# Performance work log

Hardware: AMD Instinct MI355X
Metric: run time of the kernel (lower is better)

The kernel has to match this reference:

```python
import jax, jax.numpy as jnp
import numpy as np

TOP_K = 4  # config.num_experts_per_tok


def setup_inputs() -> dict:
    key = jax.random.key(0)
    ks = jax.random.split(key, 8)
    B, S, H = 1, 2048, 1024
    E, I = 16, 512          # n_routed_experts, moe_intermediate_size
    SI = 512 * 2            # shared expert intermediate = moe_inter * n_shared_experts
    w = 0.02                # weight init scale
    return {
        "hidden_states": jax.random.normal(ks[0], (B, S, H), jnp.float32),
        "gate_w": jax.random.normal(ks[1], (E, H), jnp.float32) * w,
        "expert_gate": jax.random.normal(ks[2], (E, H, I), jnp.float32) * w,
        "expert_up": jax.random.normal(ks[3], (E, H, I), jnp.float32) * w,
        "expert_down": jax.random.normal(ks[4], (E, I, H), jnp.float32) * w,
        "shared_gate": jax.random.normal(ks[5], (H, SI), jnp.float32) * w,
        "shared_up": jax.random.normal(ks[6], (H, SI), jnp.float32) * w,
        "shared_down": jax.random.normal(ks[7], (SI, H), jnp.float32) * w,
    }


def reference(hidden_states, gate_w, expert_gate, expert_up, expert_down,
              shared_gate, shared_up, shared_down):
    B, S, H = hidden_states.shape
    E = gate_w.shape[0]
    x = hidden_states.reshape(-1, H)                     # [T, H]
    T = x.shape[0]

    # ---- MoEGate: sigmoid scores, top-k, normalize weights ----
    scores = jax.nn.sigmoid(x @ gate_w.T)                # [T, E]
    topk_w, topk_idx = jax.lax.top_k(scores, TOP_K)      # [T, k]
    topk_w = topk_w / (topk_w.sum(-1, keepdims=True) + 1e-20)

    # dense combine matrix: combine[t, e] = sum_k topk_w[t,k] * (topk_idx[t,k]==e)
    combine = jnp.zeros((T, E), x.dtype).at[
        jnp.arange(T)[:, None], topk_idx].add(topk_w)    # [T, E]

    # ---- routed experts (SwiGLU), computed densely and masked by combine ----
    g = jax.nn.silu(jnp.einsum('th,ehi->tei', x, expert_gate))
    u = jnp.einsum('th,ehi->tei', x, expert_up)
    expert_out = jnp.einsum('tei,eih->teh', g * u, expert_down)  # [T, E, H]
    y = jnp.einsum('te,teh->th', combine, expert_out)    # weighted combine

    # ---- shared expert (SwiGLU on all tokens) ----
    sg = jax.nn.silu(x @ shared_gate)
    shared_out = (sg * (x @ shared_up)) @ shared_down    # [T, H]

    return (y + shared_out).reshape(B, S, H)
```

## Files before the change

kernel.cpp:

```cpp
#include <hip/hip_runtime.h>


#define T_TOK 2048
#define H_DIM 1024
#define E_NUM 16
#define I_DIM 512
#define SI_DIM 1024

typedef __bf16 bf16x8 __attribute__((ext_vector_type(8)));
typedef short short8 __attribute__((ext_vector_type(8)));
typedef float f32x4 __attribute__((ext_vector_type(4)));
typedef unsigned short u16;

struct alignas(8) U16x4 { u16 x, y, z, w; };
struct alignas(4) U16x2 { u16 x, y; };

__device__ __forceinline__ float bf2f(u16 u) {
    union { float f; unsigned int i; } v; v.i = ((unsigned int)u) << 16; return v.f;
}
__device__ __forceinline__ u16 f2bf(float f) {
    union { float f; unsigned int i; } v; v.f = f;
    unsigned int i = v.i;
    return (u16)((i + 0x7fffu + ((i >> 16) & 1u)) >> 16);
}

#define GLOAD16(g, l)                                                          \
    __builtin_amdgcn_global_load_lds(                                          \
        (const __attribute__((address_space(1))) unsigned int*)(const void*)(g),\
        (__attribute__((address_space(3))) unsigned int*)(void*)(l), 16, 0, 0)

#define CNT(e) ((e) * 16)

__global__ __launch_bounds__(256) void route_kernel(
    const float* __restrict__ x, const float* __restrict__ gw,
    int* __restrict__ cnt, int* __restrict__ tok,
    int* __restrict__ slot, float* __restrict__ wgt)
{
    const int wid  = threadIdx.x >> 6;
    const int lane = threadIdx.x & 63;
    const int t    = blockIdx.x * 4 + wid;

    const float* xp = x + (long)t * H_DIM;
    float xr[16];
#pragma unroll
    for (int j = 0; j < 16; ++j) xr[j] = xp[lane + 64 * j];

    float sc[E_NUM];
#pragma unroll
    for (int e = 0; e < E_NUM; ++e) {
        const float* gp = gw + e * H_DIM;
        float d = 0.f;
#pragma unroll
        for (int j = 0; j < 16; ++j) d += xr[j] * gp[lane + 64 * j];
#pragma unroll
        for (int off = 32; off; off >>= 1) d += __shfl_xor(d, off);
        sc[e] = 1.f / (1.f + expf(-d));
    }

    float w[4]; int id[4];
    unsigned picked = 0;
    float sum = 0.f;
#pragma unroll
    for (int k = 0; k < 4; ++k) {
        float mv = -1.f; int mi = 0;
#pragma unroll
        for (int e = 0; e < E_NUM; ++e) {
            bool ok = !((picked >> e) & 1u) && (sc[e] > mv);
            mv = ok ? sc[e] : mv;
            mi = ok ? e : mi;
        }
        w[k] = mv; id[k] = mi; picked |= 1u << mi; sum += mv;
    }
    const float inv = 1.f / (sum + 1e-20f);

    if (lane == 0) {
#pragma unroll
        for (int k = 0; k < 4; ++k) {
            int pos = atomicAdd(&cnt[CNT(id[k])], 1);
            tok[id[k] * T_TOK + pos] = t;
            slot[t * 4 + k] = (id[k] << 16) | pos;
            wgt[t * 4 + k]  = w[k] * inv;
        }
    }
}

__global__ void scan_kernel(const int* __restrict__ cnt, int* __restrict__ ebase)
{
    if (threadIdx.x == 0) {
        int s = 0;
        for (int e = 0; e < E_NUM; ++e) { ebase[e] = s; s += cnt[CNT(e)]; }
    }
}

__global__ __launch_bounds__(256) void convert_kernel(
    const float* __restrict__ in, u16* __restrict__ out)
{
    const int i = (blockIdx.x * 256 + threadIdx.x) * 4;
    float4 v = *(const float4*)&in[i];
    U16x4 o = { f2bf(v.x), f2bf(v.y), f2bf(v.z), f2bf(v.w) };
    *(U16x4*)&out[i] = o;
}

__global__ __launch_bounds__(256) void transpose_cv(
    const float* __restrict__ in, u16* __restrict__ out, int R, int C)
{
    __shared__ float tl[64][65];
    const long boff = (long)blockIdx.z * R * C;
    const int r0 = blockIdx.y * 64, c0 = blockIdx.x * 64;
    const int tid = threadIdx.x;

#pragma unroll
    for (int p = 0; p < 16; ++p) {
        int row = p * 4 + (tid >> 6), col = tid & 63;
        tl[row][col] = in[boff + (long)(r0 + row) * C + (c0 + col)];
    }
    __syncthreads();
#pragma unroll
    for (int p = 0; p < 8; ++p) {
        int cc = p * 8 + (tid >> 5), rp = (tid & 31) * 2;
        U16x2 o = { f2bf(tl[rp][cc]), f2bf(tl[rp + 1][cc]) };
        *(U16x2*)&out[boff + (long)(c0 + cc) * R + (r0 + rp)] = o;
    }
}

template<bool DUAL, bool GATHER, bool OUTF32>
__global__ __launch_bounds__(256) void gemm_bf16(
    const u16* __restrict__ A, const u16* __restrict__ B1,
    const u16* __restrict__ B2, void* __restrict__ Out,
    const int* __restrict__ cnt, const int* __restrict__ ebase,
    const int* __restrict__ tok, int Mfixed, int K, int Ntot, long sB)
{
    const int e  = blockIdx.z;
    const int M  = cnt ? cnt[CNT(e)] : Mfixed;
    const int m0 = blockIdx.y * 128;
    if (m0 >= M) return;
    const int n0 = blockIdx.x * 64;
    const int rbase = ebase ? ebase[e] : 0;
    const u16* b1p = B1 + (long)e * sB;
    const u16* b2p = DUAL ? (B2 + (long)e * sB) : B1;

    __shared__ __attribute__((aligned(16))) u16 sA[128 * 64];
    __shared__ __attribute__((aligned(16))) u16 sB1t[64 * 64];
    __shared__ __attribute__((aligned(16))) u16 sB2t[DUAL ? 64 * 64 : 8];

    const int tid  = threadIdx.x;
    const int lane = tid & 63;
    const int wid  = tid >> 6;
    const int wr   = wid >> 1;
    const int wc   = wid & 1;

    const u16* aptr[4];
#pragma unroll
    for (int i = 0; i < 4; ++i) {
        int q = i * 256 + tid;
        int row = q >> 3, s = q & 7;
        int r = m0 + row; if (r >= M) r = M - 1;
        long grow = GATHER ? (long)tok[e * T_TOK + r] : (long)(rbase + r);
        aptr[i] = A + grow * K + ((s ^ (row & 7)) << 3);
    }
    const u16* bptr1[2]; const u16* bptr2[2];
#pragma unroll
    for (int i = 0; i < 2; ++i) {
        int q = i * 256 + tid;
        int row = q >> 3, s = q & 7;
        long go = (long)(n0 + row) * K + ((s ^ (row & 7)) << 3);
        bptr1[i] = b1p + go;
        bptr2[i] = b2p + go;
    }

    f32x4 accG[4][2], accU[4][2];
#pragma unroll
    for (int i = 0; i < 4; ++i)
#pragma unroll
        for (int j = 0; j < 2; ++j) {
            accG[i][j] = (f32x4){0.f, 0.f, 0.f, 0.f};
            if (DUAL) accU[i][j] = (f32x4){0.f, 0.f, 0.f, 0.f};
        }

    for (int kt = 0; kt < K; kt += 64) {
        __syncthreads();
#pragma unroll
        for (int i = 0; i < 4; ++i) GLOAD16(aptr[i] + kt, &sA[(i * 256 + tid) * 8]);
#pragma unroll
        for (int i = 0; i < 2; ++i) {
            GLOAD16(bptr1[i] + kt, &sB1t[(i * 256 + tid) * 8]);
            if (DUAL) GLOAD16(bptr2[i] + kt, &sB2t[(i * 256 + tid) * 8]);
        }
        asm volatile("s_waitcnt vmcnt(0)" ::: "memory");
        __syncthreads();

#pragma unroll
        for (int ks = 0; ks < 2; ++ks) {
            bf16x8 a[4], bg[2], bu[2];
#pragma unroll
            for (int mf = 0; mf < 4; ++mf) {
                int row = wr * 64 + mf * 16 + (lane & 15);
                int c   = ks * 4 + (lane >> 4);
                a[mf] = __builtin_bit_cast(bf16x8,
                    *(const short8*)&sA[row * 64 + ((c ^ (row & 7)) << 3)]);
            }
#pragma unroll
            for (int nf = 0; nf < 2; ++nf) {
                int row = wc * 32 + nf * 16 + (lane & 15);
                int c   = ks * 4 + (lane >> 4);
                int o   = row * 64 + ((c ^ (row & 7)) << 3);
                bg[nf] = __builtin_bit_cast(bf16x8, *(const short8*)&sB1t[o]);
                if (DUAL) bu[nf] = __builtin_bit_cast(bf16x8, *(const short8*)&sB2t[o]);
            }
#pragma unroll
            for (int mf = 0; mf < 4; ++mf)
#pragma unroll
                for (int nf = 0; nf < 2; ++nf) {
                    accG[mf][nf] = __builtin_amdgcn_mfma_f32_16x16x32_bf16(
                        a[mf], bg[nf], accG[mf][nf], 0, 0, 0);
                    if (DUAL)
                        accU[mf][nf] = __builtin_amdgcn_mfma_f32_16x16x32_bf16(
                            a[mf], bu[nf], accU[mf][nf], 0, 0, 0);
                }
        }
    }

#pragma unroll
    for (int mf = 0; mf < 4; ++mf)
#pragma unroll
        for (int nf = 0; nf < 2; ++nf)
#pragma unroll
            for (int r = 0; r < 4; ++r) {
                int row = m0 + wr * 64 + mf * 16 + (lane >> 4) * 4 + r;
                if (row >= M) continue;
                int col = n0 + wc * 32 + nf * 16 + (lane & 15);
                float v = accG[mf][nf][r];
                if constexpr (DUAL) {
                    float uu = accU[mf][nf][r];
                    v = v / (1.f + expf(-v)) * uu;
                }
                long oidx = (long)(rbase + row) * Ntot + col;
                if constexpr (OUTF32) ((float*)Out)[oidx] = v;
                else                  ((u16*)Out)[oidx]   = f2bf(v);
            }
}

__global__ __launch_bounds__(256) void combine_kernel(
    float* __restrict__ out, const u16* __restrict__ pair,
    const int* __restrict__ slot, const float* __restrict__ wgt,
    const int* __restrict__ ebase)
{
    const int t = blockIdx.x;
    const int c = threadIdx.x * 4;
    float4 o = *(float4*)&out[(long)t * H_DIM + c];
#pragma unroll
    for (int k = 0; k < 4; ++k) {
        int s = slot[t * 4 + k];
        int e = s >> 16, pos = s & 0xffff;
        float w = wgt[t * 4 + k];
        const u16* pr = pair + (long)(ebase[e] + pos) * H_DIM + c;
        U16x4 pv = *(const U16x4*)pr;
        o.x += w * bf2f(pv.x);
        o.y += w * bf2f(pv.y);
        o.z += w * bf2f(pv.z);
        o.w += w * bf2f(pv.w);
    }
    *(float4*)&out[(long)t * H_DIM + c] = o;
}

extern "C" void kernel_launch(void* const* d_in, const int* in_sizes, int n_in,
                              void* d_out, int out_size, void* d_ws, size_t ws_size,
                              hipStream_t stream)
{
    const float* x  = (const float*)d_in[0];
    const float* gw = (const float*)d_in[1];
    const float* eg = (const float*)d_in[2];
    const float* eu = (const float*)d_in[3];
    const float* ed = (const float*)d_in[4];
    const float* sg = (const float*)d_in[5];
    const float* su = (const float*)d_in[6];
    const float* sd = (const float*)d_in[7];
    float* out = (float*)d_out;

    unsigned char* w = (unsigned char*)d_ws;
    size_t off = 0;
    auto alloc = [&](size_t b) -> void* {
        off = (off + 255) & ~(size_t)255;
        void* p = w + off; off += b; return p;
    };
    int*   cnt   = (int*)  alloc(256 * 4);
    int*   ebase = (int*)  alloc(16 * 4);
    int*   tok   = (int*)  alloc((size_t)E_NUM * T_TOK * 4);
    int*   slot  = (int*)  alloc((size_t)T_TOK * 4 * 4);
    float* wgt   = (float*)alloc((size_t)T_TOK * 4 * 4);
    u16*   xb    = (u16*)  alloc((size_t)T_TOK * H_DIM * 2);
    u16*   egT   = (u16*)  alloc((size_t)E_NUM * I_DIM * H_DIM * 2);
    u16*   euT   = (u16*)  alloc((size_t)E_NUM * I_DIM * H_DIM * 2);
    u16*   edT   = (u16*)  alloc((size_t)E_NUM * H_DIM * I_DIM * 2);
    u16*   sgT   = (u16*)  alloc((size_t)SI_DIM * H_DIM * 2);
    u16*   suT   = (u16*)  alloc((size_t)SI_DIM * H_DIM * 2);
    u16*   sdT   = (u16*)  alloc((size_t)H_DIM * SI_DIM * 2);
    u16*   actR  = (u16*)  alloc((size_t)T_TOK * 4 * I_DIM * 2);
    u16*   actS  = (u16*)  alloc((size_t)T_TOK * SI_DIM * 2);
    u16*   pair  = (u16*)  alloc((size_t)T_TOK * 4 * H_DIM * 2);

    hipMemsetAsync(cnt, 0, 256 * 4, stream);

    route_kernel<<<T_TOK / 4, 256, 0, stream>>>(x, gw, cnt, tok, slot, wgt);
    scan_kernel<<<1, 64, 0, stream>>>(cnt, ebase);

    convert_kernel<<<T_TOK * H_DIM / 1024, 256, 0, stream>>>(x, xb);
    transpose_cv<<<dim3(I_DIM / 64, H_DIM / 64, E_NUM), 256, 0, stream>>>(eg, egT, H_DIM, I_DIM);
    transpose_cv<<<dim3(I_DIM / 64, H_DIM / 64, E_NUM), 256, 0, stream>>>(eu, euT, H_DIM, I_DIM);
    transpose_cv<<<dim3(H_DIM / 64, I_DIM / 64, E_NUM), 256, 0, stream>>>(ed, edT, I_DIM, H_DIM);
    transpose_cv<<<dim3(16, 16, 1), 256, 0, stream>>>(sg, sgT, H_DIM, SI_DIM);
    transpose_cv<<<dim3(16, 16, 1), 256, 0, stream>>>(su, suT, H_DIM, SI_DIM);
    transpose_cv<<<dim3(16, 16, 1), 256, 0, stream>>>(sd, sdT, SI_DIM, H_DIM);

    gemm_bf16<true, true, false><<<dim3(I_DIM / 64, 16, E_NUM), 256, 0, stream>>>(
        xb, egT, euT, actR, cnt, ebase, tok, 0, H_DIM, I_DIM, (long)I_DIM * H_DIM);
    gemm_bf16<true, false, false><<<dim3(SI_DIM / 64, T_TOK / 128, 1), 256, 0, stream>>>(
        xb, sgT, suT, actS, nullptr, nullptr, nullptr, T_TOK, H_DIM, SI_DIM, 0);
    gemm_bf16<false, false, false><<<dim3(H_DIM / 64, 16, E_NUM), 256, 0, stream>>>(
        actR, edT, nullptr, pair, cnt, ebase, nullptr, 0, I_DIM, H_DIM, (long)H_DIM * I_DIM);
    gemm_bf16<false, false, true><<<dim3(H_DIM / 64, T_TOK / 128, 1), 256, 0, stream>>>(
        actS, sdT, nullptr, out, nullptr, nullptr, nullptr, T_TOK, SI_DIM, H_DIM, 0);

    combine_kernel<<<T_TOK, 256, 0, stream>>>(out, pair, slot, wgt, ebase);
}
```

Before: 291.0 us.

## Merge launches into fused transpose and grouped GEMM kernels with double-buffered LDS

Measured after the change: 351.4 us. +20.8%, slower.

```diff
diff --git a/kernel.cpp b/kernel.cpp
--- a/kernel.cpp
+++ b/kernel.cpp
@@ -34,7 +34,7 @@
 __global__ __launch_bounds__(256) void route_kernel(
     const float* __restrict__ x, const float* __restrict__ gw,
     int* __restrict__ cnt, int* __restrict__ tok,
-    int* __restrict__ slot, float* __restrict__ wgt)
+    int* __restrict__ slot, float* __restrict__ wgt, u16* __restrict__ xb)
 {
     const int wid  = threadIdx.x >> 6;
     const int lane = threadIdx.x & 63;
@@ -44,6 +44,9 @@
     float xr[16];
 #pragma unroll
     for (int j = 0; j < 16; ++j) xr[j] = xp[lane + 64 * j];
+
+#pragma unroll
+    for (int j = 0; j < 16; ++j) xb[(long)t * H_DIM + lane + 64 * j] = f2bf(xr[j]);
 
     float sc[E_NUM];
 #pragma unroll
@@ -84,29 +87,13 @@
     }
 }
 
-__global__ void scan_kernel(const int* __restrict__ cnt, int* __restrict__ ebase)
-{
-    if (threadIdx.x == 0) {
-        int s = 0;
-        for (int e = 0; e < E_NUM; ++e) { ebase[e] = s; s += cnt[CNT(e)]; }
-    }
-}
-
-__global__ __launch_bounds__(256) void convert_kernel(
-    const float* __restrict__ in, u16* __restrict__ out)
-{
-    const int i = (blockIdx.x * 256 + threadIdx.x) * 4;
-    float4 v = *(const float4*)&in[i];
-    U16x4 o = { f2bf(v.x), f2bf(v.y), f2bf(v.z), f2bf(v.w) };
-    *(U16x4*)&out[i] = o;
-}
-
-__global__ __launch_bounds__(256) void transpose_cv(
-    const float* __restrict__ in, u16* __restrict__ out, int R, int C)
+__device__ __forceinline__ void tr_tile(
+    const float* __restrict__ in, u16* __restrict__ out,
+    int R, int C, int z, int by, int bx)
 {
     __shared__ float tl[64][65];
-    const long boff = (long)blockIdx.z * R * C;
-    const int r0 = blockIdx.y * 64, c0 = blockIdx.x * 64;
+    const long boff = (long)z * R * C;
+    const int r0 = by * 64, c0 = bx * 64;
     const int tid = threadIdx.x;
 
 #pragma unroll
@@ -123,25 +110,90 @@
     }
 }
 
-template<bool DUAL, bool GATHER, bool OUTF32>
-__global__ __launch_bounds__(256) void gemm_bf16(
-    const u16* __restrict__ A, const u16* __restrict__ B1,
-    const u16* __restrict__ B2, void* __restrict__ Out,
-    const int* __restrict__ cnt, const int* __restrict__ ebase,
-    const int* __restrict__ tok, int Mfixed, int K, int Ntot, long sB)
-{
-    const int e  = blockIdx.z;
-    const int M  = cnt ? cnt[CNT(e)] : Mfixed;
-    const int m0 = blockIdx.y * 128;
+__global__ __launch_bounds__(256) void transpose_mega(
+    const float* __restrict__ eg, const float* __restrict__ eu,
+    const float* __restrict__ ed, const float* __restrict__ sg,
+    const float* __restrict__ su, const float* __restrict__ sd,
+    u16* __restrict__ egT, u16* __restrict__ euT, u16* __restrict__ edT,
+    u16* __restrict__ sgT, u16* __restrict__ suT, u16* __restrict__ sdT)
+{
+    int b = blockIdx.x;
+    if (b < 2048) {
+        int z = b >> 7, rem = b & 127;
+        tr_tile(eg, egT, H_DIM, I_DIM, z, rem >> 3, rem & 7);
+    } else if (b < 4096) {
+        int l = b - 2048; int z = l >> 7, rem = l & 127;
+        tr_tile(eu, euT, H_DIM, I_DIM, z, rem >> 3, rem & 7);
+    } else if (b < 6144) {
+        int l = b - 4096; int z = l >> 7, rem = l & 127;
+        tr_tile(ed, edT, I_DIM, H_DIM, z, rem >> 4, rem & 15);
+    } else if (b < 6400) {
+        int l = b - 6144;
+        tr_tile(sg, sgT, H_DIM, SI_DIM, 0, l >> 4, l & 15);
+    } else if (b < 6656) {
+        int l = b - 6400;
+        tr_tile(su, suT, H_DIM, SI_DIM, 0, l >> 4, l & 15);
+    } else {
+        int l = b - 6656;
+        tr_tile(sd, sdT, SI_DIM, H_DIM, 0, l >> 4, l & 15);
+    }
+}
+
+template<int MODE>
+__global__ __launch_bounds__(256) void gemm_moe(
+    const u16* __restrict__ xb, const u16* __restrict__ actR,
+    const u16* __restrict__ actS,
+    const u16* __restrict__ Wr1, const u16* __restrict__ Wr2,
+    const u16* __restrict__ Ws1, const u16* __restrict__ Ws2,
+    u16* __restrict__ outR, void* __restrict__ outS,
+    const int* __restrict__ cnt, const int* __restrict__ tok)
+{
+    constexpr bool DUAL  = (MODE == 0);
+    constexpr int  NWG   = (MODE == 0) ? 2304 : 4352;
+    constexpr int  CPX   = NWG / 8;
+    constexpr int  RB    = (MODE == 0) ? 2048 : 4096;
+    constexpr int  PER_E = RB / E_NUM;
+
+    const int bswz = blockIdx.x;
+    const int idx  = (bswz & 7) * CPX + (bswz >> 3);
+
+    const bool routed = idx < RB;
+    int e = 0, mb, nb;
+    if (routed) {
+        e = idx / PER_E;
+        int rem = idx % PER_E;
+        nb = rem >> 4;
+        mb = rem & 15;
+    } else {
+        int rem = idx - RB;
+        nb = rem >> 4;
+        mb = rem & 15;
+    }
+
+    int M, K, Ntot, rbase = 0;
+    const u16 *Ap, *B1p, *B2p = nullptr;
+    if (routed) {
+        M = cnt[CNT(e)];
+#pragma unroll
+        for (int i = 0; i < E_NUM; ++i) rbase += (i < e) ? cnt[CNT(i)] : 0;
+        K    = (MODE == 0) ? H_DIM : I_DIM;
+        Ntot = (MODE == 0) ? I_DIM : H_DIM;
+        Ap   = (MODE == 0) ? xb : actR;
+        B1p  = Wr1 + (long)e * (512L * 1024L);
+        if (DUAL) B2p = Wr2 + (long)e * (512L * 1024L);
+    } else {
+        M = T_TOK; K = (MODE == 0) ? H_DIM : SI_DIM;
+        Ntot = (MODE == 0) ? SI_DIM : H_DIM;
+        Ap = (MODE == 0) ? xb : actS;
+        B1p = Ws1; if (DUAL) B2p = Ws2;
+    }
+    const int m0 = mb * 128;
     if (m0 >= M) return;
-    const int n0 = blockIdx.x * 64;
-    const int rbase = ebase ? ebase[e] : 0;
-    const u16* b1p = B1 + (long)e * sB;
-    const u16* b2p = DUAL ? (B2 + (long)e * sB) : B1;
-
-    __shared__ __attribute__((aligned(16))) u16 sA[128 * 64];
-    __shared__ __attribute__((aligned(16))) u16 sB1t[64 * 64];
-    __shared__ __attribute__((aligned(16))) u16 sB2t[DUAL ? 64 * 64 : 8];
+    const int n0 = nb * 64;
+
+    __shared__ __attribute__((aligned(16))) u16 sA[2][128 * 64];
+    __shared__ __attribute__((aligned(16))) u16 sB1[2][64 * 64];
+    __shared__ __attribute__((aligned(16))) u16 sB2[DUAL ? 2 : 1][DUAL ? 64 * 64 : 8];
 
     const int tid  = threadIdx.x;
     const int lane = tid & 63;
@@ -155,8 +207,11 @@
         int q = i * 256 + tid;
         int row = q >> 3, s = q & 7;
         int r = m0 + row; if (r >= M) r = M - 1;
-        long grow = GATHER ? (long)tok[e * T_TOK + r] : (long)(rbase + r);
-        aptr[i] = A + grow * K + ((s ^ (row & 7)) << 3);
+        long grow;
+        if (MODE == 0 && routed) grow = tok[e * T_TOK + r];
+        else if (routed)         grow = rbase + r;
+        else                     grow = r;
+        aptr[i] = Ap + grow * (long)K + ((s ^ (row & 7)) << 3);
     }
     const u16* bptr1[2]; const u16* bptr2[2];
 #pragma unroll
@@ -164,8 +219,8 @@
         int q = i * 256 + tid;
         int row = q >> 3, s = q & 7;
         long go = (long)(n0 + row) * K + ((s ^ (row & 7)) << 3);
-        bptr1[i] = b1p + go;
-        bptr2[i] = b2p + go;
+        bptr1[i] = B1p + go;
+        bptr2[i] = DUAL ? (B2p + go) : B1p;
     }
 
     f32x4 accG[4][2], accU[4][2];
@@ -177,18 +232,28 @@
             if (DUAL) accU[i][j] = (f32x4){0.f, 0.f, 0.f, 0.f};
         }
 
-    for (int kt = 0; kt < K; kt += 64) {
-        __syncthreads();
-#pragma unroll
-        for (int i = 0; i < 4; ++i) GLOAD16(aptr[i] + kt, &sA[(i * 256 + tid) * 8]);
+    auto STAGE = [&](int buf, int kt) {
+#pragma unroll
+        for (int i = 0; i < 4; ++i) GLOAD16(aptr[i] + kt, &sA[buf][(i * 256 + tid) * 8]);
 #pragma unroll
         for (int i = 0; i < 2; ++i) {
-            GLOAD16(bptr1[i] + kt, &sB1t[(i * 256 + tid) * 8]);
-            if (DUAL) GLOAD16(bptr2[i] + kt, &sB2t[(i * 256 + tid) * 8]);
-        }
-        asm volatile("s_waitcnt vmcnt(0)" ::: "memory");
-        __syncthreads();
-
+            GLOAD16(bptr1[i] + kt, &sB1[buf][(i * 256 + tid) * 8]);
+            if (DUAL) GLOAD16(bptr2[i] + kt, &sB2[buf][(i * 256 + tid) * 8]);
+        }
+    };
+
+    const int nt = K >> 6;
+    STAGE(0, 0);
+    asm volatile("s_waitcnt vmcnt(0)" ::: "memory");
+    __syncthreads();
+
+    int cur = 0;
+    for (int t = 0; t < nt; ++t) {
+        if (t + 1 < nt) STAGE(cur ^ 1, (t + 1) << 6);
+
+        const u16* sAc  = sA[cur];
+        const u16* sB1c = sB1[cur];
+        const u16* sB2c = sB2[DUAL ? cur : 0];
 #pragma unroll
         for (int ks = 0; ks < 2; ++ks) {
             bf16x8 a[4], bg[2], bu[2];
@@ -197,15 +262,15 @@
                 int row = wr * 64 + mf * 16 + (lane & 15);
                 int c   = ks * 4 + (lane >> 4);
                 a[mf] = __builtin_bit_cast(bf16x8,
-                    *(const short8*)&sA[row * 64 + ((c ^ (row & 7)) << 3)]);
+                    *(const short8*)&sAc[row * 64 + ((c ^ (row & 7)) << 3)]);
             }
 #pragma unroll
             for (int nf = 0; nf < 2; ++nf) {
                 int row = wc * 32 + nf * 16 + (lane & 15);
                 int c   = ks * 4 + (lane >> 4);
                 int o   = row * 64 + ((c ^ (row & 7)) << 3);
-                bg[nf] = __builtin_bit_cast(bf16x8, *(const short8*)&sB1t[o]);
-                if (DUAL) bu[nf] = __builtin_bit_cast(bf16x8, *(const short8*)&sB2t[o]);
+                bg[nf] = __builtin_bit_cast(bf16x8, *(const short8*)&sB1c[o]);
+                if (DUAL) bu[nf] = __builtin_bit_cast(bf16x8, *(const short8*)&sB2c[o]);
             }
 #pragma unroll
             for (int mf = 0; mf < 4; ++mf)
@@ -218,6 +283,12 @@
                             a[mf], bu[nf], accU[mf][nf], 0, 0, 0);
                 }
         }
+
+        if (t + 1 < nt) {
+            asm volatile("s_waitcnt vmcnt(0)" ::: "memory");
+            __syncthreads();
+        }
+        cur ^= 1;
     }
 
 #pragma unroll
@@ -234,17 +305,26 @@
                     float uu = accU[mf][nf][r];
                     v = v / (1.f + expf(-v)) * uu;
                 }
-                long oidx = (long)(rbase + row) * Ntot + col;
-                if constexpr (OUTF32) ((float*)Out)[oidx] = v;
-                else                  ((u16*)Out)[oidx]   = f2bf(v);
+                long orow = routed ? (long)(rbase + row) : (long)row;
+                if (MODE == 1 && !routed) ((float*)outS)[orow * Ntot + col] = v;
+                else if (routed)          outR[orow * Ntot + col] = f2bf(v);
+                else                      ((u16*)outS)[orow * Ntot + col] = f2bf(v);
             }
 }
 
 __global__ __launch_bounds__(256) void combine_kernel(
     float* __restrict__ out, const u16* __restrict__ pair,
     const int* __restrict__ slot, const float* __restrict__ wgt,
-    const int* __restrict__ ebase)
-{
+    const int* __restrict__ cnt)
+{
+    __shared__ int eb_s[E_NUM];
+    if (threadIdx.x < E_NUM) {
+        int s = 0;
+        for (int i = 0; i < E_NUM; ++i) s += (i < (int)threadIdx.x) ? cnt[CNT(i)] : 0;
+        eb_s[threadIdx.x] = s;
+    }
+    __syncthreads();
+
     const int t = blockIdx.x;
     const int c = threadIdx.x * 4;
     float4 o = *(float4*)&out[(long)t * H_DIM + c];
@@ -253,7 +333,7 @@
         int s = slot[t * 4 + k];
         int e = s >> 16, pos = s & 0xffff;
         float w = wgt[t * 4 + k];
-        const u16* pr = pair + (long)(ebase[e] + pos) * H_DIM + c;
+        const u16* pr = pair + (long)(eb_s[e] + pos) * H_DIM + c;
         U16x4 pv = *(const U16x4*)pr;
         o.x += w * bf2f(pv.x);
         o.y += w * bf2f(pv.y);
@@ -283,43 +363,31 @@
         off = (off + 255) & ~(size_t)255;
         void* p = w + off; off += b; return p;
     };
-    int*   cnt   = (int*)  alloc(256 * 4);
-    int*   ebase = (int*)  alloc(16 * 4);
-    int*   tok   = (int*)  alloc((size_t)E_NUM * T_TOK * 4);
-    int*   slot  = (int*)  alloc((size_t)T_TOK * 4 * 4);
-    float* wgt   = (float*)alloc((size_t)T_TOK * 4 * 4);
-    u16*   xb    = (u16*)  alloc((size_t)T_TOK * H_DIM * 2);
-    u16*   egT   = (u16*)  alloc((size_t)E_NUM * I_DIM * H_DIM * 2);
-    u16*   euT   = (u16*)  alloc((size_t)E_NUM * I_DIM * H_DIM * 2);
-    u16*   edT   = (u16*)  alloc((size_t)E_NUM * H_DIM * I_DIM * 2);
-    u16*   sgT   = (u16*)  alloc((size_t)SI_DIM * H_DIM * 2);
-    u16*   suT   = (u16*)  alloc((size_t)SI_DIM * H_DIM * 2);
-    u16*   sdT   = (u16*)  alloc((size_t)H_DIM * SI_DIM * 2);
-    u16*   actR  = (u16*)  alloc((size_t)T_TOK * 4 * I_DIM * 2);
-    u16*   actS  = (u16*)  alloc((size_t)T_TOK * SI_DIM * 2);
-    u16*   pair  = (u16*)  alloc((size_t)T_TOK * 4 * H_DIM * 2);
+    int*   cnt  = (int*)  alloc(256 * 4);
+    int*   tok  = (int*)  alloc((size_t)E_NUM * T_TOK * 4);
+    int*   slot = (int*)  alloc((size_t)T_TOK * 4 * 4);
+    float* wgt  = (float*)alloc((size_t)T_TOK * 4 * 4);
+    u16*   xb   = (u16*)  alloc((size_t)T_TOK * H_DIM * 2);
+    u16*   egT  = (u16*)  alloc((size_t)E_NUM * I_DIM * H_DIM * 2);
+    u16*   euT  = (u16*)  alloc((size_t)E_NUM * I_DIM * H_DIM * 2);
+    u16*   edT  = (u16*)  alloc((size_t)E_NUM * H_DIM * I_DIM * 2);
+    u16*   sgT  = (u16*)  alloc((size_t)SI_DIM * H_DIM * 2);
+    u16*   suT  = (u16*)  alloc((size_t)SI_DIM * H_DIM * 2);
+    u16*   sdT  = (u16*)  alloc((size_t)H_DIM * SI_DIM * 2);
+    u16*   actR = (u16*)  alloc((size_t)T_TOK * 4 * I_DIM * 2);
+    u16*   actS = (u16*)  alloc((size_t)T_TOK * SI_DIM * 2);
+    u16*   pair = (u16*)  alloc((size_t)T_TOK * 4 * H_DIM * 2);
 
     hipMemsetAsync(cnt, 0, 256 * 4, stream);
 
-    route_kernel<<<T_TOK / 4, 256, 0, stream>>>(x, gw, cnt, tok, slot, wgt);
-    scan_kernel<<<1, 64, 0, stream>>>(cnt, ebase);
-
-    convert_kernel<<<T_TOK * H_DIM / 1024, 256, 0, stream>>>(x, xb);
-    transpose_cv<<<dim3(I_DIM / 64, H_DIM / 64, E_NUM), 256, 0, stream>>>(eg, egT, H_DIM, I_DIM);
-    transpose_cv<<<dim3(I_DIM / 64, H_DIM / 64, E_NUM), 256, 0, stream>>>(eu, euT, H_DIM, I_DIM);
-    transpose_cv<<<dim3(H_DIM / 64, I_DIM / 64, E_NUM), 256, 0, stream>>>(ed, edT, I_DIM, H_DIM);
-    transpose_cv<<<dim3(16, 16, 1), 256, 0, stream>>>(sg, sgT, H_DIM, SI_DIM);
-    transpose_cv<<<dim3(16, 16, 1), 256, 0, stream>>>(su, suT, H_DIM, SI_DIM);
-    transpose_cv<<<dim3(16, 16, 1), 256, 0, stream>>>(sd, sdT, SI_DIM, H_DIM);
-
-    gemm_bf16<true, true, false><<<dim3(I_DIM / 64, 16, E_NUM), 256, 0, stream>>>(
-        xb, egT, euT, actR, cnt, ebase, tok, 0, H_DIM, I_DIM, (long)I_DIM * H_DIM);
-    gemm_bf16<true, false, false><<<dim3(SI_DIM / 64, T_TOK / 128, 1), 256, 0, stream>>>(
-        xb, sgT, suT, actS, nullptr, nullptr, nullptr, T_TOK, H_DIM, SI_DIM, 0);
-    gemm_bf16<false, false, false><<<dim3(H_DIM / 64, 16, E_NUM), 256, 0, stream>>>(
-        actR, edT, nullptr, pair, cnt, ebase, nullptr, 0, I_DIM, H_DIM, (long)H_DIM * I_DIM);
-    gemm_bf16<false, false, true><<<dim3(H_DIM / 64, T_TOK / 128, 1), 256, 0, stream>>>(
-        actS, sdT, nullptr, out, nullptr, nullptr, nullptr, T_TOK, SI_DIM, H_DIM, 0);
-
-    combine_kernel<<<T_TOK, 256, 0, stream>>>(out, pair, slot, wgt, ebase);
-}
+    route_kernel<<<T_TOK / 4, 256, 0, stream>>>(x, gw, cnt, tok, slot, wgt, xb);
+    transpose_mega<<<6912, 256, 0, stream>>>(eg, eu, ed, sg, su, sd,
+                                             egT, euT, edT, sgT, suT, sdT);
+    gemm_moe<0><<<2304, 256, 0, stream>>>(xb, nullptr, nullptr,
+                                          egT, euT, sgT, suT,
+                                          actR, actS, cnt, tok);
+    gemm_moe<1><<<4352, 256, 0, stream>>>(nullptr, actR, actS,
+                                          edT, nullptr, sdT, nullptr,
+                                          pair, out, cnt, nullptr);
+    combine_kernel<<<T_TOK, 256, 0, stream>>>(out, pair, slot, wgt, cnt);
+}
```
